# Kernel optimization log

Measured on AMD Instinct MI355X. Metric: run time of the kernel, lower is better.

The kernel has to match this reference:

```python
import jax, jax.numpy as jnp
import numpy as np

EPS = 1e-9
CAPACITY_FACTOR = 1.25
MIN_EXPERT_CAPACITY = 4
SECOND_THRESHOLD = 0.2
LOSS_COEF = 0.01

B, N, D, E, H = 4, 2048, 1024, 16, 4096


def setup_inputs() -> dict:
    key = jax.random.key(0)
    k_x, k_g, k_w1, k_w2, k_n = jax.random.split(key, 5)
    return {
        "x": jax.random.normal(k_x, (B, N, D), dtype=jnp.float32),
        "w_gating": jax.random.normal(k_g, (D, E), dtype=jnp.float32) * 0.02,
        "w1": jax.random.normal(k_w1, (E, D, H), dtype=jnp.float32) * 0.02,
        "w2": jax.random.normal(k_w2, (E, H, D), dtype=jnp.float32) * 0.02,
        "noise": jax.random.uniform(k_n, (B, N), dtype=jnp.float32),
    }


def top2_gating(x, w_gating, noise):
    b, n, d = x.shape
    e = w_gating.shape[1]
    # static expert capacity (training-mode capacity factor)
    capacity = max(min(n, int((n * CAPACITY_FACTOR) / e)), MIN_EXPERT_CAPACITY)
    raw_gates = jax.nn.softmax(jnp.einsum('bnd,de->bne', x, w_gating), axis=-1)  # [b,n,e]

    index_1 = jnp.argmax(raw_gates, axis=-1)                     # [b,n]
    mask_1 = jax.nn.one_hot(index_1, e, dtype=raw_gates.dtype)   # [b,n,e]
    gate_1 = jnp.max(raw_gates, axis=-1)                         # [b,n]

    gates_wo1 = raw_gates * (1.0 - mask_1)
    index_2 = jnp.argmax(gates_wo1, axis=-1)
    mask_2 = jax.nn.one_hot(index_2, e, dtype=raw_gates.dtype)
    gate_2 = jnp.max(gates_wo1, axis=-1)

    denom = gate_1 + gate_2 + EPS
    gate_1 = gate_1 / denom
    gate_2 = gate_2 / denom

    # second policy == 'random': keep second expert with prob gate_2 / threshold
    keep_2 = (noise < gate_2 / max(SECOND_THRESHOLD, EPS)).astype(raw_gates.dtype)
    mask_2 = mask_2 * keep_2[..., None]

    # load-balancing auxiliary loss
    density_1 = jnp.mean(mask_1, axis=-2)          # [b,e]
    density_proxy = jnp.mean(raw_gates, axis=-2)   # [b,e]
    loss = jnp.mean(density_proxy * density_1) * float(e * e)

    # position of each token within its primary expert (exclusive cumsum)
    pos_1 = (jnp.cumsum(mask_1, axis=-2) - mask_1) * mask_1
    mask_1 = mask_1 * (pos_1 < capacity).astype(raw_gates.dtype)
    mask_1_count = jnp.sum(mask_1, axis=-2, keepdims=True)
    mask_1_flat = jnp.sum(mask_1, axis=-1)
    pos_1 = jnp.sum(pos_1, axis=-1).astype(jnp.int32)  # [b,n]
    gate_1 = gate_1 * mask_1_flat

    pos_2 = (jnp.cumsum(mask_2, axis=-2) - mask_2 + mask_1_count) * mask_2
    mask_2 = mask_2 * (pos_2 < capacity).astype(raw_gates.dtype)
    mask_2_flat = jnp.sum(mask_2, axis=-1)
    pos_2 = jnp.sum(pos_2, axis=-1).astype(jnp.int32)
    gate_2 = gate_2 * mask_2_flat

    # one_hot of out-of-range positions yields zeros == safe_one_hot[..., :capacity]
    combine = (
        gate_1[..., None, None] * mask_1_flat[..., None, None]
        * jax.nn.one_hot(index_1, e, dtype=raw_gates.dtype)[..., None]
        * jax.nn.one_hot(pos_1, capacity, dtype=raw_gates.dtype)[..., None, :]
        + gate_2[..., None, None] * mask_2_flat[..., None, None]
        * jax.nn.one_hot(index_2, e, dtype=raw_gates.dtype)[..., None]
        * jax.nn.one_hot(pos_2, capacity, dtype=raw_gates.dtype)[..., None, :]
    )  # [b,n,e,c]
    dispatch = (combine != 0).astype(combine.dtype)
    return dispatch, combine, loss


def reference(x, w_gating, w1, w2, noise):
    dispatch, combine, loss = top2_gating(x, w_gating, noise)
    expert_inputs = jnp.einsum('bnd,bnec->ebcd', x, dispatch)  # [e,b,c,d]
    e, b, c, d = expert_inputs.shape
    ei = expert_inputs.reshape(e, b * c, d)
    hidden = jax.nn.relu(jnp.einsum('etd,edh->eth', ei, w1))
    eo = jnp.einsum('eth,ehd->etd', hidden, w2).reshape(e, b, c, d)
    output = jnp.einsum('ebcd,bnec->bnd', eo, combine)
    return output, loss * LOSS_COEF
```

## Files before the change

kernel.cpp:

```cpp
#include <hip/hip_runtime.h>

#define BB 4
#define NT_TOK 2048
#define DD 1024
#define EE 16
#define HH 4096
#define CAP 160
#define NTOK (BB * NT_TOK)
#define MROWS (BB * CAP)

typedef __attribute__((ext_vector_type(4))) float floatx4;
typedef __attribute__((ext_vector_type(8))) short short8;

__device__ __forceinline__ ushort f2bf(float f) {
  union { float f; unsigned u; } v; v.f = f;
  unsigned u = v.u;
  return (ushort)((u + 0x7FFFu + ((u >> 16) & 1u)) >> 16);
}

__device__ __forceinline__ uint cvt_pk_bf16(float lo, float hi) {
  uint r;
  asm("v_cvt_pk_bf16_f32 %0, %1, %2" : "=v"(r) : "v"(lo), "v"(hi));
  return r;
}

__device__ __forceinline__ void gload_lds16(const void* g, void* l) {
  __builtin_amdgcn_global_load_lds(
      (const __attribute__((address_space(1))) unsigned*)g,
      (__attribute__((address_space(3))) unsigned*)l, 16, 0, 0);
}

__global__ __launch_bounds__(256)
void k_gating(const float* __restrict__ x, const float* __restrict__ wg,
              const float* __restrict__ noise,
              int* __restrict__ idx1, int* __restrict__ idx2,
              float* __restrict__ g1, float* __restrict__ g2,
              int* __restrict__ pos1, int* __restrict__ pos2,
              float* __restrict__ dp, float* __restrict__ d1)
{
  __shared__ float s_dp[EE];
  __shared__ float s_d1[EE];
  const int tid = threadIdx.x, lane = tid & 63, wave = tid >> 6;
  if (tid < EE) { s_dp[tid] = 0.f; s_d1[tid] = 0.f; }
  __syncthreads();

  const int t = blockIdx.x * 4 + wave;
  const int b = t / NT_TOK;

  float acc[EE];
#pragma unroll
  for (int e = 0; e < EE; ++e) acc[e] = 0.f;

  const float* xr = x + (size_t)t * DD;
#pragma unroll 4
  for (int i = 0; i < DD / 64; ++i) {
    const int d = i * 64 + lane;
    const float xv = xr[d];
    const float4* wr = (const float4*)(wg + (size_t)d * EE);
#pragma unroll
    for (int q = 0; q < 4; ++q) {
      const float4 w4 = wr[q];
      acc[q * 4 + 0] += xv * w4.x;
      acc[q * 4 + 1] += xv * w4.y;
      acc[q * 4 + 2] += xv * w4.z;
      acc[q * 4 + 3] += xv * w4.w;
    }
  }
#pragma unroll
  for (int off = 32; off >= 1; off >>= 1)
#pragma unroll
    for (int e = 0; e < EE; ++e) acc[e] += __shfl_xor(acc[e], off);

  float mx = acc[0];
#pragma unroll
  for (int e = 1; e < EE; ++e) mx = fmaxf(mx, acc[e]);
  float g[EE], s = 0.f;
#pragma unroll
  for (int e = 0; e < EE; ++e) { g[e] = expf(acc[e] - mx); s += g[e]; }
  const float inv = 1.f / s;
#pragma unroll
  for (int e = 0; e < EE; ++e) g[e] *= inv;

  int i1 = 0; float v1 = g[0];
#pragma unroll
  for (int e = 1; e < EE; ++e) if (g[e] > v1) { v1 = g[e]; i1 = e; }
  int i2 = -1; float v2 = -1.f;
#pragma unroll
  for (int e = 0; e < EE; ++e) if (e != i1 && g[e] > v2) { v2 = g[e]; i2 = e; }

  const float denom = v1 + v2 + 1e-9f;
  const float g1n = v1 / denom, g2n = v2 / denom;
  const bool keep2 = noise[t] < (g2n / 0.2f);

  if (lane == 0) {
    idx1[t] = i1;
    idx2[t] = keep2 ? i2 : -1;
    g1[t] = g1n; g2[t] = g2n;
    pos1[t] = -1; pos2[t] = -1;
  }
  if (lane < EE) atomicAdd(&s_dp[lane], g[lane]);
  if (lane == 0) atomicAdd(&s_d1[i1], 1.f);
  __syncthreads();
  if (tid < EE) {
    atomicAdd(&dp[b * EE + tid], s_dp[tid]);
    atomicAdd(&d1[b * EE + tid], s_d1[tid]);
  }
}

__global__ __launch_bounds__(64)
void k_scan(const int* __restrict__ idx1, const int* __restrict__ idx2,
            int* __restrict__ pos1, int* __restrict__ pos2,
            int* __restrict__ slot_tok)
{
  const int b = (int)blockIdx.x >> 4;
  const int e = (int)blockIdx.x & 15;
  const int lane = threadIdx.x;
  const unsigned long long lm = (1ull << lane) - 1ull;
  int* st = slot_tok + ((size_t)e * BB + b) * CAP;

  int v[NT_TOK / 64];
#pragma unroll
  for (int c = 0; c < NT_TOK / 64; ++c) v[c] = idx1[b * NT_TOK + c * 64 + lane];
  int base = 0;
  for (int c = 0; c < NT_TOK / 64; ++c) {
    const bool m = (v[c] == e);
    const unsigned long long bal = __ballot(m);
    if (m) {
      const int p = base + __popcll(bal & lm);
      if (p < CAP) { const int n = c * 64 + lane; pos1[b * NT_TOK + n] = p; st[p] = n; }
    }
    base += __popcll(bal);
  }
  const int count1 = base < CAP ? base : CAP;

#pragma unroll
  for (int c = 0; c < NT_TOK / 64; ++c) v[c] = idx2[b * NT_TOK + c * 64 + lane];
  base = count1;
  for (int c = 0; c < NT_TOK / 64; ++c) {
    const bool m = (v[c] == e);
    const unsigned long long bal = __ballot(m);
    if (m) {
      const int p = base + __popcll(bal & lm);
      if (p < CAP) { const int n = c * 64 + lane; pos2[b * NT_TOK + n] = p; st[p] = n; }
    }
    base += __popcll(bal);
  }
  const int used = base < CAP ? base : CAP;
  for (int p = used + lane; p < CAP; p += 64) st[p] = -1;
}

__global__ __launch_bounds__(256)
void k_gather(const float* __restrict__ x, const int* __restrict__ slot_tok,
              ushort* __restrict__ ei)
{
  const int s = blockIdx.x;
  const int tid = threadIdx.x;
  const int r = s % MROWS;
  const int b = r / CAP;
  const int tok = slot_tok[s];
  ushort4 o;
  if (tok >= 0) {
    const float4 v = *(const float4*)(x + ((size_t)b * NT_TOK + tok) * DD + tid * 4);
    o.x = f2bf(v.x); o.y = f2bf(v.y); o.z = f2bf(v.z); o.w = f2bf(v.w);
  } else {
    o.x = 0; o.y = 0; o.z = 0; o.w = 0;
  }
  *(ushort4*)(ei + (size_t)s * DD + tid * 4) = o;
}

template<int K, int NC, bool RELU_BF16>
__global__ __launch_bounds__(256)
void expert_gemm(const ushort* __restrict__ A, const float* __restrict__ W,
                 ushort* __restrict__ Cb, float* __restrict__ Cf)
{
  constexpr int MT = MROWS / 128;
  constexpr int NTl = NC / 128;
  constexpr int nwg = EE * MT * NTl;
  constexpr int NKT = K / 32;
  int wg = ((int)blockIdx.x & 7) * (nwg / 8) + ((int)blockIdx.x >> 3);
  const int mt = wg % MT; wg /= MT;
  const int nt = wg % NTl;
  const int e  = wg / NTl;
  const int m0 = mt * 128, n0 = nt * 128;

  __shared__ ushort As[2][128 * 32];
  __shared__ ushort Bs[2][128 * 32];

  const int tid = threadIdx.x;
  const int lane = tid & 63;
  const int wv = tid >> 6;
  const int wr = wv >> 1;
  const int wc = wv & 1;
  const int fr = lane & 15, fq = lane >> 4;

  const ushort* Ae = A + (size_t)e * MROWS * K;
  const float*  We = W + (size_t)e * K * NC;

  const int arow = wv * 32 + (lane >> 2);
  const int lchunk = (lane & 3) ^ ((arow >> 1) & 3);
  const ushort* Ag0 = Ae + (size_t)(m0 + arow) * K + lchunk * 8;
  const ushort* Ag1 = Ag0 + (size_t)16 * K;
  const int n_loc = tid & 127;
  const int kc = tid >> 7;
  const float* Wb = We + n0 + n_loc;
  const int bswz0 = n_loc * 32 + (((kc)     ^ ((n_loc >> 1) & 3)) << 3);
  const int bswz1 = n_loc * 32 + (((kc + 2) ^ ((n_loc >> 1) & 3)) << 3);
  const int cswr = (fq ^ ((fr >> 1) & 3)) << 3;

  floatx4 acc[4][4];
#pragma unroll
  for (int m = 0; m < 4; ++m)
#pragma unroll
    for (int n = 0; n < 4; ++n) acc[m][n] = (floatx4){0.f, 0.f, 0.f, 0.f};

  float bq0[8], bq1[8];

  auto issue_A = [&](int kt, int buf) {
    gload_lds16(Ag0 + kt * 32, (void*)&As[buf][(wv * 32) * 32]);
    gload_lds16(Ag1 + kt * 32, (void*)&As[buf][(wv * 32 + 16) * 32]);
  };
  auto load_B = [&](int kt) {
    const float* p0 = Wb + (size_t)(kt * 32 + kc * 8) * NC;
    const float* p1 = Wb + (size_t)(kt * 32 + (kc + 2) * 8) * NC;
#pragma unroll
    for (int j = 0; j < 8; ++j) bq0[j] = p0[(size_t)j * NC];
#pragma unroll
    for (int j = 0; j < 8; ++j) bq1[j] = p1[(size_t)j * NC];
  };
  auto write_B = [&](int buf) {
    ushort* bs_ = Bs[buf];
    uint4 q;
    q.x = cvt_pk_bf16(bq0[0], bq0[1]); q.y = cvt_pk_bf16(bq0[2], bq0[3]);
    q.z = cvt_pk_bf16(bq0[4], bq0[5]); q.w = cvt_pk_bf16(bq0[6], bq0[7]);
    *(uint4*)&bs_[bswz0] = q;
    q.x = cvt_pk_bf16(bq1[0], bq1[1]); q.y = cvt_pk_bf16(bq1[2], bq1[3]);
    q.z = cvt_pk_bf16(bq1[4], bq1[5]); q.w = cvt_pk_bf16(bq1[6], bq1[7]);
    *(uint4*)&bs_[bswz1] = q;
  };

  issue_A(0, 0);
  load_B(0);
  write_B(0);
  __syncthreads();

  for (int kt = 0; kt < NKT; ++kt) {
    const int cur = kt & 1;
    const bool more = (kt + 1 < NKT);
    if (more) { issue_A(kt + 1, cur ^ 1); load_B(kt + 1); }

    const ushort* as_ = As[cur];
    const ushort* bs_ = Bs[cur];
    short8 af[4], bfr[4];
#pragma unroll
    for (int m = 0; m < 4; ++m)
      af[m] = *(const short8*)&as_[(wr * 64 + m * 16 + fr) * 32 + cswr];
#pragma unroll
    for (int n = 0; n < 4; ++n)
      bfr[n] = *(const short8*)&bs_[(wc * 64 + n * 16 + fr) * 32 + cswr];
#pragma unroll
    for (int m = 0; m < 4; ++m)
#pragma unroll
      for (int n = 0; n < 4; ++n)
        acc[m][n] = __builtin_amdgcn_mfma_f32_16x16x32_bf16(af[m], bfr[n], acc[m][n], 0, 0, 0);

    if (more) {
      write_B(cur ^ 1);
      __syncthreads();
    }
  }

#pragma unroll
  for (int m = 0; m < 4; ++m) {
    const int row0 = m0 + wr * 64 + m * 16 + fq * 4;
#pragma unroll
    for (int n = 0; n < 4; ++n) {
      const int col = n0 + wc * 64 + n * 16 + fr;
#pragma unroll
      for (int j = 0; j < 4; ++j) {
        const size_t ci = ((size_t)e * MROWS + row0 + j) * NC + col;
        if constexpr (RELU_BF16) Cb[ci] = f2bf(fmaxf(acc[m][n][j], 0.f));
        else                     Cf[ci] = acc[m][n][j];
      }
    }
  }
}

__global__ __launch_bounds__(256)
void k_combine(const float* __restrict__ eo,
               const int* __restrict__ idx1, const int* __restrict__ idx2,
               const float* __restrict__ g1, const float* __restrict__ g2,
               const int* __restrict__ pos1, const int* __restrict__ pos2,
               float* __restrict__ out)
{
  const int t = blockIdx.x, tid = threadIdx.x;
  const int b = t / NT_TOK;
  float r0 = 0.f, r1 = 0.f, r2 = 0.f, r3 = 0.f;
  const int p1 = pos1[t];
  if (p1 >= 0) {
    const float g = g1[t];
    const float4 v = *(const float4*)(eo + ((size_t)idx1[t] * MROWS + b * CAP + p1) * DD + tid * 4);
    r0 += g * v.x; r1 += g * v.y; r2 += g * v.z; r3 += g * v.w;
  }
  const int p2 = pos2[t];
  if (p2 >= 0) {
    const float g = g2[t];
    const float4 v = *(const float4*)(eo + ((size_t)idx2[t] * MROWS + b * CAP + p2) * DD + tid * 4);
    r0 += g * v.x; r1 += g * v.y; r2 += g * v.z; r3 += g * v.w;
  }
  float4 o; o.x = r0; o.y = r1; o.z = r2; o.w = r3;
  *(float4*)(out + (size_t)t * DD + tid * 4) = o;
}

__global__ __launch_bounds__(64)
void k_loss(const float* __restrict__ dens, float* __restrict__ out_loss)
{
  const int lane = threadIdx.x;
  float v = (dens[lane] * (1.f / 2048.f)) * (dens[64 + lane] * (1.f / 2048.f));
#pragma unroll
  for (int off = 32; off >= 1; off >>= 1) v += __shfl_xor(v, off);
  if (lane == 0) out_loss[0] = (v / 64.f) * 256.f * 0.01f;
}

extern "C" void kernel_launch(void* const* d_in, const int* in_sizes, int n_in,
                              void* d_out, int out_size, void* d_ws, size_t ws_size,
                              hipStream_t stream)
{
  const float* x     = (const float*)d_in[0];
  const float* wgate = (const float*)d_in[1];
  const float* w1    = (const float*)d_in[2];
  const float* w2    = (const float*)d_in[3];
  const float* noise = (const float*)d_in[4];
  float* out = (float*)d_out;

  size_t off = 0;
  char* wsb = (char*)d_ws;
  auto alloc = [&](size_t bytes) -> void* {
    void* p = wsb + off;
    off += (bytes + 255) & ~(size_t)255;
    return p;
  };
  ushort* ei  = (ushort*)alloc((size_t)EE * MROWS * DD * 2);
  ushort* hid = (ushort*)alloc((size_t)EE * MROWS * HH * 2);
  float*  eo  = (float*) alloc((size_t)EE * MROWS * DD * 4);
  int*   idx1 = (int*)  alloc((size_t)NTOK * 4);
  int*   idx2 = (int*)  alloc((size_t)NTOK * 4);
  float* g1   = (float*)alloc((size_t)NTOK * 4);
  float* g2   = (float*)alloc((size_t)NTOK * 4);
  int*   pos1 = (int*)  alloc((size_t)NTOK * 4);
  int*   pos2 = (int*)  alloc((size_t)NTOK * 4);
  int* slot_tok = (int*)alloc((size_t)EE * BB * CAP * 4);
  float* dens = (float*)alloc(128 * 4);

  hipMemsetAsync(dens, 0, 128 * 4, stream);
  k_gating<<<NTOK / 4, 256, 0, stream>>>(x, wgate, noise, idx1, idx2, g1, g2,
                                         pos1, pos2, dens, dens + 64);
  k_scan<<<BB * EE, 64, 0, stream>>>(idx1, idx2, pos1, pos2, slot_tok);
  k_gather<<<EE * MROWS, 256, 0, stream>>>(x, slot_tok, ei);
  expert_gemm<DD, HH, true ><<<EE * (MROWS / 128) * (HH / 128), 256, 0, stream>>>(ei,  w1, hid, nullptr);
  expert_gemm<HH, DD, false><<<EE * (MROWS / 128) * (DD / 128), 256, 0, stream>>>(hid, w2, nullptr, eo);
  k_combine<<<NTOK, 256, 0, stream>>>(eo, idx1, idx2, g1, g2, pos1, pos2, out);
  k_loss<<<1, 64, 0, stream>>>(dens, out + (size_t)NTOK * DD);
}
```

Baseline: 464.4 us.

## Pre-transpose expert weights to bf16 and load both GEMM operands directly into LDS

Adds a kernel that converts each expert weight matrix to bf16 in an N-major (transposed) layout before each GEMM. The GEMM then loads B tiles with the same direct global-to-LDS path as A, instead of loading fp32 into registers, converting and writing to LDS. This removes the conversion work and register staging from the main loop and halves the bytes of each repeated weight read. In exchange, it adds an extra pass over the full weights with poorly coalesced transposed writes, plus a large workspace buffer.

```diff
diff --git a/kernel.cpp b/kernel.cpp
--- a/kernel.cpp
+++ b/kernel.cpp
@@ -168,9 +168,32 @@
   *(ushort4*)(ei + (size_t)s * DD + tid * 4) = o;
 }
 
+template<int K, int NC>
+__global__ __launch_bounds__(256)
+void k_convT(const float* __restrict__ W, ushort* __restrict__ T)
+{
+  constexpr int KT = K / 32, NT2 = NC / 64;
+  int bbx = blockIdx.x;
+  const int kt = bbx % KT; bbx /= KT;
+  const int nt = bbx % NT2;
+  const int e  = bbx / NT2;
+  const int tid = threadIdx.x;
+  const int n  = nt * 64 + (tid & 63);
+  const int k0 = kt * 32 + (tid >> 6) * 8;
+
+  const float* p = W + ((size_t)e * K + k0) * NC + n;
+  float w[8];
+#pragma unroll
+  for (int j = 0; j < 8; ++j) w[j] = p[(size_t)j * NC];
+  uint4 q;
+  q.x = cvt_pk_bf16(w[0], w[1]); q.y = cvt_pk_bf16(w[2], w[3]);
+  q.z = cvt_pk_bf16(w[4], w[5]); q.w = cvt_pk_bf16(w[6], w[7]);
+  *(uint4*)(T + ((size_t)e * NC + n) * K + k0) = q;
+}
+
 template<int K, int NC, bool RELU_BF16>
 __global__ __launch_bounds__(256)
-void expert_gemm(const ushort* __restrict__ A, const float* __restrict__ W,
+void expert_gemm(const ushort* __restrict__ A, const ushort* __restrict__ BT,
                  ushort* __restrict__ Cb, float* __restrict__ Cf)
 {
   constexpr int MT = MROWS / 128;
@@ -189,22 +212,20 @@
   const int tid = threadIdx.x;
   const int lane = tid & 63;
   const int wv = tid >> 6;
-  const int wr = wv >> 1;
-  const int wc = wv & 1;
+  const int wr = wv >> 1, wc = wv & 1;
   const int fr = lane & 15, fq = lane >> 4;
 
-  const ushort* Ae = A + (size_t)e * MROWS * K;
-  const float*  We = W + (size_t)e * K * NC;
+  const ushort* Ae = A  + (size_t)e * MROWS * K;
+  const ushort* Be = BT + (size_t)e * NC * K;
 
   const int arow = wv * 32 + (lane >> 2);
-  const int lchunk = (lane & 3) ^ ((arow >> 1) & 3);
-  const ushort* Ag0 = Ae + (size_t)(m0 + arow) * K + lchunk * 8;
+  const int achk = (lane & 3) ^ ((arow >> 1) & 3);
+  const ushort* Ag0 = Ae + (size_t)(m0 + arow) * K + achk * 8;
   const ushort* Ag1 = Ag0 + (size_t)16 * K;
-  const int n_loc = tid & 127;
-  const int kc = tid >> 7;
-  const float* Wb = We + n0 + n_loc;
-  const int bswz0 = n_loc * 32 + (((kc)     ^ ((n_loc >> 1) & 3)) << 3);
-  const int bswz1 = n_loc * 32 + (((kc + 2) ^ ((n_loc >> 1) & 3)) << 3);
+  const ushort* Bg0 = Be + (size_t)(n0 + arow) * K + achk * 8;
+  const ushort* Bg1 = Bg0 + (size_t)16 * K;
+  const int dst0 = (wv * 32) * 32;
+  const int dst1 = (wv * 32 + 16) * 32;
   const int cswr = (fq ^ ((fr >> 1) & 3)) << 3;
 
   floatx4 acc[4][4];
@@ -213,40 +234,21 @@
 #pragma unroll
     for (int n = 0; n < 4; ++n) acc[m][n] = (floatx4){0.f, 0.f, 0.f, 0.f};
 
-  float bq0[8], bq1[8];
-
-  auto issue_A = [&](int kt, int buf) {
-    gload_lds16(Ag0 + kt * 32, (void*)&As[buf][(wv * 32) * 32]);
-    gload_lds16(Ag1 + kt * 32, (void*)&As[buf][(wv * 32 + 16) * 32]);
+  auto issue = [&](int kt, int buf) {
+    const size_t ko = (size_t)kt * 32;
+    gload_lds16(Ag0 + ko, (void*)&As[buf][dst0]);
+    gload_lds16(Ag1 + ko, (void*)&As[buf][dst1]);
+    gload_lds16(Bg0 + ko, (void*)&Bs[buf][dst0]);
+    gload_lds16(Bg1 + ko, (void*)&Bs[buf][dst1]);
   };
-  auto load_B = [&](int kt) {
-    const float* p0 = Wb + (size_t)(kt * 32 + kc * 8) * NC;
-    const float* p1 = Wb + (size_t)(kt * 32 + (kc + 2) * 8) * NC;
-#pragma unroll
-    for (int j = 0; j < 8; ++j) bq0[j] = p0[(size_t)j * NC];
-#pragma unroll
-    for (int j = 0; j < 8; ++j) bq1[j] = p1[(size_t)j * NC];
-  };
-  auto write_B = [&](int buf) {
-    ushort* bs_ = Bs[buf];
-    uint4 q;
-    q.x = cvt_pk_bf16(bq0[0], bq0[1]); q.y = cvt_pk_bf16(bq0[2], bq0[3]);
-    q.z = cvt_pk_bf16(bq0[4], bq0[5]); q.w = cvt_pk_bf16(bq0[6], bq0[7]);
-    *(uint4*)&bs_[bswz0] = q;
-    q.x = cvt_pk_bf16(bq1[0], bq1[1]); q.y = cvt_pk_bf16(bq1[2], bq1[3]);
-    q.z = cvt_pk_bf16(bq1[4], bq1[5]); q.w = cvt_pk_bf16(bq1[6], bq1[7]);
-    *(uint4*)&bs_[bswz1] = q;
-  };
-
-  issue_A(0, 0);
-  load_B(0);
-  write_B(0);
+
+  issue(0, 0);
   __syncthreads();
 
   for (int kt = 0; kt < NKT; ++kt) {
     const int cur = kt & 1;
     const bool more = (kt + 1 < NKT);
-    if (more) { issue_A(kt + 1, cur ^ 1); load_B(kt + 1); }
+    if (more) issue(kt + 1, cur ^ 1);
 
     const ushort* as_ = As[cur];
     const ushort* bs_ = Bs[cur];
@@ -263,10 +265,7 @@
       for (int n = 0; n < 4; ++n)
         acc[m][n] = __builtin_amdgcn_mfma_f32_16x16x32_bf16(af[m], bfr[n], acc[m][n], 0, 0, 0);
 
-    if (more) {
-      write_B(cur ^ 1);
-      __syncthreads();
-    }
+    if (more) __syncthreads();
   }
 
 #pragma unroll
@@ -342,6 +341,7 @@
   ushort* ei  = (ushort*)alloc((size_t)EE * MROWS * DD * 2);
   ushort* hid = (ushort*)alloc((size_t)EE * MROWS * HH * 2);
   float*  eo  = (float*) alloc((size_t)EE * MROWS * DD * 4);
+  ushort* wbT = (ushort*)alloc((size_t)EE * DD * HH * 2);
   int*   idx1 = (int*)  alloc((size_t)NTOK * 4);
   int*   idx2 = (int*)  alloc((size_t)NTOK * 4);
   float* g1   = (float*)alloc((size_t)NTOK * 4);
@@ -356,8 +356,10 @@
                                          pos1, pos2, dens, dens + 64);
   k_scan<<<BB * EE, 64, 0, stream>>>(idx1, idx2, pos1, pos2, slot_tok);
   k_gather<<<EE * MROWS, 256, 0, stream>>>(x, slot_tok, ei);
-  expert_gemm<DD, HH, true ><<<EE * (MROWS / 128) * (HH / 128), 256, 0, stream>>>(ei,  w1, hid, nullptr);
-  expert_gemm<HH, DD, false><<<EE * (MROWS / 128) * (DD / 128), 256, 0, stream>>>(hid, w2, nullptr, eo);
+  k_convT<DD, HH><<<EE * (HH / 64) * (DD / 32), 256, 0, stream>>>(w1, wbT);
+  expert_gemm<DD, HH, true ><<<EE * (MROWS / 128) * (HH / 128), 256, 0, stream>>>(ei,  wbT, hid, nullptr);
+  k_convT<HH, DD><<<EE * (DD / 64) * (HH / 32), 256, 0, stream>>>(w2, wbT);
+  expert_gemm<HH, DD, false><<<EE * (MROWS / 128) * (DD / 128), 256, 0, stream>>>(hid, wbT, nullptr, eo);
   k_combine<<<NTOK, 256, 0, stream>>>(eo, idx1, idx2, g1, g2, pos1, pos2, out);
   k_loss<<<1, 64, 0, stream>>>(dens, out + (size_t)NTOK * DD);
 }
```

Result: slower. 626.2 us (+34.8%).
